# Kernel optimization log

Measured on AMD Instinct MI355X. Metric: run time of the kernel, lower is better.

The kernel has to match this reference:

```python
import jax, jax.numpy as jnp
import numpy as np

OBS, ACT, HID, MIX, TOPK = 64, 16, 256, 16, 4
EPS = 1e-5

def _ln(x, g, b):
    m = jnp.mean(x, axis=-1, keepdims=True)
    v = jnp.mean(jnp.square(x - m), axis=-1, keepdims=True)
    return (x - m) * jax.lax.rsqrt(v + EPS) * g + b

def setup_inputs() -> dict:
    key = jax.random.key(0)
    ks = jax.random.split(key, 12)
    B = 16384
    D = OBS + ACT            # 80
    F = HID * MIX            # 4096
    s = lambda fan_in: 1.0 / np.sqrt(fan_in)
    return {
        "x": jax.random.normal(ks[0], (B, OBS), jnp.float32),
        "a": jax.random.normal(ks[1], (B, ACT), jnp.float32),
        "W1": jax.random.uniform(ks[2], (F, D), jnp.float32, -s(D), s(D)),
        "b1": jnp.zeros((F,), jnp.float32),
        "W2": jax.random.uniform(ks[3], (F, F), jnp.float32, -s(F), s(F)),
        "b2": jnp.zeros((F,), jnp.float32),
        "W3": jax.random.uniform(ks[4], (1, HID), jnp.float32, -s(HID), s(HID)),
        "b3": jnp.zeros((1,), jnp.float32),
        "g1": jnp.ones((F,), jnp.float32),
        "be1": jnp.zeros((F,), jnp.float32),
        "g2": jnp.ones((F,), jnp.float32),
        "be2": jnp.zeros((F,), jnp.float32),
        "Wg": jax.random.uniform(ks[5], (MIX, D), jnp.float32, -s(D), s(D)),
        "bg": jnp.zeros((MIX,), jnp.float32),
    }

def reference(x, a, W1, b1, W2, b2, W3, b3, g1, be1, g2, be2, Wg, bg):
    B = x.shape[0]
    xa = jnp.concatenate([x, a], axis=1)                      # [B, D]
    gate_scores = jax.nn.softmax(xa @ Wg.T + bg, axis=-1)     # [B, MIX]
    topk_vals, topk_idx = jax.lax.top_k(gate_scores, TOPK)    # [B, K]
    # renormalize top-k weights, scatter into dense score tensor
    topk_vals = topk_vals / jnp.sum(topk_vals, axis=-1, keepdims=True)
    scores = jnp.zeros_like(gate_scores).at[
        jnp.arange(B)[:, None], topk_idx].set(topk_vals)      # [B, MIX]
    h = jax.nn.relu(_ln(xa @ W1.T + b1, g1, be1))             # [B, HID*MIX]
    h = jax.nn.relu(_ln(h @ W2.T + b2, g2, be2))              # [B, HID*MIX]
    h = h.reshape(B, HID, MIX)                                # row-major, same as torch
    h = jnp.mean(h * scores[:, None, :], axis=-1)             # [B, HID]
    return h @ W3.T + b3                                      # [B, 1]
```

## Files before the change

kernel.cpp:

```cpp
#include <hip/hip_runtime.h>
#include <stdint.h>

#define OBS 64
#define ACTD 16
#define DIN 80
#define MIX 16
#define FF 4096
#define NB 16384
#define CHUNK 4096
#define KP 96
#define LNEPS 1e-5f

typedef float f32x4 __attribute__((ext_vector_type(4)));
typedef short bf16x8 __attribute__((ext_vector_type(8)));

__device__ __forceinline__ unsigned short f2bf(float f) {
    union { float f; uint32_t u; } v; v.f = f;
    uint32_t u = v.u;
    u += 0x7fff + ((u >> 16) & 1);
    return (unsigned short)(u >> 16);
}
__device__ __forceinline__ float bf2f(unsigned short h) {
    union { uint32_t u; float f; } v; v.u = ((uint32_t)h) << 16;
    return v.f;
}

__global__ __launch_bounds__(256) void k_conv(const float* __restrict__ W,
                                              unsigned short* __restrict__ O, int n4) {
    int i = blockIdx.x * 256 + threadIdx.x;
    if (i >= n4) return;
    float4 v = ((const float4*)W)[i];
    ushort4 o;
    o.x = f2bf(v.x); o.y = f2bf(v.y); o.z = f2bf(v.z); o.w = f2bf(v.w);
    ((ushort4*)O)[i] = o;
}

__global__ __launch_bounds__(256) void k_prep(const float* __restrict__ x, const float* __restrict__ a,
                                              const float* __restrict__ W1, const float* __restrict__ b1,
                                              unsigned short* __restrict__ xab,
                                              unsigned short* __restrict__ W1b) {
    int t = threadIdx.x;
    if (blockIdx.x < 16) {
        int row = blockIdx.x * 256 + t;
        const float4* xp = (const float4*)(x + (size_t)row * OBS);
        unsigned short* o = xab + (size_t)row * KP;
#pragma unroll
        for (int i = 0; i < 16; ++i) {
            float4 v = xp[i];
            ushort4 u; u.x = f2bf(v.x); u.y = f2bf(v.y); u.z = f2bf(v.z); u.w = f2bf(v.w);
            ((ushort4*)o)[i] = u;
        }
        const float4* ap = (const float4*)(a + (size_t)row * ACTD);
#pragma unroll
        for (int i = 0; i < 4; ++i) {
            float4 v = ap[i];
            ushort4 u; u.x = f2bf(v.x); u.y = f2bf(v.y); u.z = f2bf(v.z); u.w = f2bf(v.w);
            ((ushort4*)(o + OBS))[i] = u;
        }
        ushort4 t0; t0.x = 0x3F80; t0.y = 0; t0.z = 0; t0.w = 0;
        ushort4 z;  z.x = 0; z.y = 0; z.z = 0; z.w = 0;
        ((ushort4*)(o + 80))[0] = t0;
        ((ushort4*)(o + 84))[0] = z;
        ((ushort4*)(o + 88))[0] = z;
        ((ushort4*)(o + 92))[0] = z;
    } else {
        int f = (blockIdx.x - 16) * 256 + t;
        const float4* wp = (const float4*)(W1 + (size_t)f * DIN);
        unsigned short* o = W1b + (size_t)f * KP;
#pragma unroll
        for (int i = 0; i < 20; ++i) {
            float4 v = wp[i];
            ushort4 u; u.x = f2bf(v.x); u.y = f2bf(v.y); u.z = f2bf(v.z); u.w = f2bf(v.w);
            ((ushort4*)o)[i] = u;
        }
        ushort4 t0; t0.x = f2bf(b1[f]); t0.y = 0; t0.z = 0; t0.w = 0;
        ushort4 z;  z.x = 0; z.y = 0; z.z = 0; z.w = 0;
        ((ushort4*)(o + 80))[0] = t0;
        ((ushort4*)(o + 84))[0] = z;
        ((ushort4*)(o + 88))[0] = z;
        ((ushort4*)(o + 92))[0] = z;
    }
}

__global__ __launch_bounds__(256) void k_gate(const float* __restrict__ x, const float* __restrict__ a,
                                              const float* __restrict__ Wg, const float* __restrict__ bg,
                                              float* __restrict__ scores) {
    __shared__ float wgs[MIX * DIN];
    __shared__ float bgs[MIX];
    int t = threadIdx.x;
    for (int e = t; e < MIX * DIN; e += 256) wgs[e] = Wg[e];
    if (t < MIX) bgs[t] = bg[t];
    __syncthreads();
    int row = blockIdx.x * 256 + t;
    float xa[DIN];
    const float4* xp = (const float4*)(x + (size_t)row * OBS);
#pragma unroll
    for (int i = 0; i < OBS / 4; ++i) {
        float4 v = xp[i];
        xa[i*4] = v.x; xa[i*4+1] = v.y; xa[i*4+2] = v.z; xa[i*4+3] = v.w;
    }
    const float4* ap = (const float4*)(a + (size_t)row * ACTD);
#pragma unroll
    for (int i = 0; i < ACTD / 4; ++i) {
        float4 v = ap[i];
        xa[OBS+i*4] = v.x; xa[OBS+i*4+1] = v.y; xa[OBS+i*4+2] = v.z; xa[OBS+i*4+3] = v.w;
    }
    double p[MIX];
    double mx = -1e300;
#pragma unroll
    for (int m = 0; m < MIX; ++m) {
        double acc = (double)bgs[m];
#pragma unroll
        for (int k = 0; k < DIN; ++k) acc += (double)xa[k] * (double)wgs[m*DIN + k];
        p[m] = acc;
        if (acc > mx) mx = acc;
    }
#pragma unroll
    for (int m = 0; m < MIX; ++m) p[m] = exp(p[m] - mx);
    unsigned used = 0;
    double s4 = 0.0;
#pragma unroll
    for (int j = 0; j < 4; ++j) {
        int best = 0; double bv = -1.0;
#pragma unroll
        for (int m = 0; m < MIX; ++m)
            if (!((used >> m) & 1) && p[m] > bv) { bv = p[m]; best = m; }
        used |= 1u << best;
        s4 += bv;
    }
    float* so = scores + (size_t)row * MIX;
#pragma unroll
    for (int m = 0; m < MIX; ++m)
        so[m] = ((used >> m) & 1) ? (float)(p[m] / s4) : 0.f;
}

__global__ __launch_bounds__(256) void k_gemm1(const unsigned short* __restrict__ A,
                                               const unsigned short* __restrict__ B,
                                               unsigned short* __restrict__ C,
                                               float* __restrict__ pstats) {
    __shared__ alignas(16) unsigned short As[12288];
    __shared__ alignas(16) unsigned short Bs[12288];
    int t = threadIdx.x;
    int pm = blockIdx.x & 31;
    int pn = blockIdx.x >> 5;
    int lane = t & 63, wid = t >> 6, wm = wid >> 1, wn = wid & 1;
    int l15 = lane & 15, l4 = lane >> 4;

    const unsigned short* Ap = A + (size_t)pm * 128 * KP;
    const unsigned short* Bp = B + (size_t)pn * 128 * KP;

#pragma unroll
    for (int i = 0; i < 6; ++i) {
        int u = i * 256 + t;
        int r = u / 12, s12 = u - r * 12;
        int q = s12 >> 2, s = s12 & 3;
        int goff = r * KP + q * 32 + ((s ^ ((r >> 1) & 3)) * 8);
        __builtin_amdgcn_global_load_lds(
            (const __attribute__((address_space(1))) void*)(Ap + goff),
            (__attribute__((address_space(3))) void*)(As + u * 8), 16, 0, 0);
        __builtin_amdgcn_global_load_lds(
            (const __attribute__((address_space(1))) void*)(Bp + goff),
            (__attribute__((address_space(3))) void*)(Bs + u * 8), 16, 0, 0);
    }
    __syncthreads();

    f32x4 acc[4][4] = {};
#pragma unroll
    for (int q = 0; q < 3; ++q) {
        bf16x8 af[4], bfr[4];
#pragma unroll
        for (int mf = 0; mf < 4; ++mf) {
            int r = wm * 64 + mf * 16 + l15;
            int sl = l4 ^ ((r >> 1) & 3);
            af[mf] = *(const bf16x8*)(As + (r * 12 + q * 4 + sl) * 8);
        }
#pragma unroll
        for (int nf = 0; nf < 4; ++nf) {
            int r = wn * 64 + nf * 16 + l15;
            int sl = l4 ^ ((r >> 1) & 3);
            bfr[nf] = *(const bf16x8*)(Bs + (r * 12 + q * 4 + sl) * 8);
        }
#pragma unroll
        for (int mf = 0; mf < 4; ++mf)
#pragma unroll
            for (int nf = 0; nf < 4; ++nf)
                acc[mf][nf] = __builtin_amdgcn_mfma_f32_16x16x32_bf16(af[mf], bfr[nf], acc[mf][nf], 0, 0, 0);
    }

    int rowbase = pm * 128 + wm * 64 + l4 * 4;
#pragma unroll
    for (int mf = 0; mf < 4; ++mf) {
#pragma unroll
        for (int rr = 0; rr < 4; ++rr) {
            float ss = 0.f, qq = 0.f;
#pragma unroll
            for (int nf = 0; nf < 4; ++nf) {
                float v = acc[mf][nf][rr];
                ss += v; qq += v * v;
            }
#pragma unroll
            for (int mask = 1; mask <= 8; mask <<= 1) {
                ss += __shfl_xor(ss, mask);
                qq += __shfl_xor(qq, mask);
            }
            if (l15 == 0) {
                int row = rowbase + mf * 16 + rr;
                int j = pn * 2 + wn;
                pstats[((size_t)row * 64 + j) * 2 + 0] = ss;
                pstats[((size_t)row * 64 + j) * 2 + 1] = qq;
            }
        }
    }

    __syncthreads();
    unsigned short* tw = As + wid * 1280;
#pragma unroll
    for (int mf = 0; mf < 4; ++mf) {
#pragma unroll
        for (int nf = 0; nf < 4; ++nf)
#pragma unroll
            for (int rr = 0; rr < 4; ++rr) {
                int row16 = l4 * 4 + rr;
                int col = l15 + nf * 16;
                tw[row16 * 80 + col] = f2bf(acc[mf][nf][rr]);
            }
        asm volatile("s_waitcnt lgkmcnt(0)" ::: "memory");
        const bf16x8* rp = (const bf16x8*)(tw + (lane >> 2) * 80 + (lane & 3) * 16);
        bf16x8 v0 = rp[0];
        bf16x8 v1 = rp[1];
        int grow = pm * 128 + wm * 64 + mf * 16 + (lane >> 2);
        int gcol = pn * 128 + wn * 64 + (lane & 3) * 16;
        *(bf16x8*)(C + (size_t)grow * FF + gcol) = v0;
        *(bf16x8*)(C + (size_t)grow * FF + gcol + 8) = v1;
        asm volatile("s_waitcnt lgkmcnt(0)" ::: "memory");
    }
}

__global__ __launch_bounds__(256) void k_ln1(unsigned short* __restrict__ h1,
                                             const float* __restrict__ pstats,
                                             const float* __restrict__ g1, const float* __restrict__ be1) {
    __shared__ float st[8][2];
    int t = threadIdx.x;
    int r0 = blockIdx.x * 8;
    if (t < 8) {
        float s = 0.f, q = 0.f;
        const float* pp = pstats + (size_t)(r0 + t) * 128;
#pragma unroll
        for (int j = 0; j < 64; ++j) { s += pp[j * 2]; q += pp[j * 2 + 1]; }
        float mu = s / (float)FF;
        float var = q / (float)FF - mu * mu;
        st[t][0] = mu;
        st[t][1] = rsqrtf(var + LNEPS);
    }
    __syncthreads();
    int c = t * 16;
    float g[16], b[16];
#pragma unroll
    for (int q = 0; q < 4; ++q) {
        float4 gv = *(const float4*)(g1 + c + q * 4);
        float4 bv = *(const float4*)(be1 + c + q * 4);
        g[q*4] = gv.x; g[q*4+1] = gv.y; g[q*4+2] = gv.z; g[q*4+3] = gv.w;
        b[q*4] = bv.x; b[q*4+1] = bv.y; b[q*4+2] = bv.z; b[q*4+3] = bv.w;
    }
    for (int r = 0; r < 8; ++r) {
        float mu = st[r][0], rs = st[r][1];
        unsigned short* hp = h1 + (size_t)(r0 + r) * FF + c;
        uint4 u0 = *(const uint4*)hp;
        uint4 u1 = *(const uint4*)(hp + 8);
        uint32_t uu[8] = {u0.x, u0.y, u0.z, u0.w, u1.x, u1.y, u1.z, u1.w};
        uint32_t oo[8];
#pragma unroll
        for (int q = 0; q < 8; ++q) {
            float v0 = bf2f((unsigned short)(uu[q] & 0xffff));
            float v1 = bf2f((unsigned short)(uu[q] >> 16));
            float o0 = fmaxf((v0 - mu) * rs * g[q*2]   + b[q*2],   0.f);
            float o1 = fmaxf((v1 - mu) * rs * g[q*2+1] + b[q*2+1], 0.f);
            oo[q] = (uint32_t)f2bf(o0) | ((uint32_t)f2bf(o1) << 16);
        }
        uint4 w0; w0.x = oo[0]; w0.y = oo[1]; w0.z = oo[2]; w0.w = oo[3];
        uint4 w1; w1.x = oo[4]; w1.y = oo[5]; w1.z = oo[6]; w1.w = oo[7];
        *(uint4*)hp = w0;
        *(uint4*)(hp + 8) = w1;
    }
}

__global__ __launch_bounds__(512, 1) void k_gemm2(const unsigned short* __restrict__ A,
                                                  const unsigned short* __restrict__ B,
                                                  unsigned short* __restrict__ C) {
    constexpr int K = FF;
    constexpr int NKT = K / 64;
    __shared__ alignas(16) unsigned short As[2][2][8192];
    __shared__ alignas(16) unsigned short Bs[2][2][8192];

    int t = threadIdx.x;
    int lane = t & 63, wid = t >> 6;
    int wm = wid >> 2, wn = wid & 3;

    int bid = blockIdx.x;
    int xcd = bid & 7, w = bid >> 3;
    int pm = (xcd >> 1) * 4 + (w >> 3);
    int pn = (xcd & 1) * 8 + (w & 7);

    const unsigned short* Ap = A + (size_t)pm * 256 * K;
    const unsigned short* Bp = B + (size_t)pn * 256 * K;

    int l15 = lane & 15, l4 = lane >> 4;
    int slk0 = (l4 ^ (l15 & 7)) * 16;
    int slk1 = ((4 + l4) ^ (l15 & 7)) * 16;
    const char* Abase = (const char*)&As[0][0][0];
    const char* Bbase = (const char*)&Bs[0][0][0];
    const char* afp0 = Abase + wm * 16384 + l15 * 128 + slk0;
    const char* afp1 = Abase + wm * 16384 + l15 * 128 + slk1;
    const char* bfp0 = Bbase + (wn >> 1) * 16384 + (wn & 1) * 8192 + l15 * 128 + slk0;
    const char* bfp1 = Bbase + (wn >> 1) * 16384 + (wn & 1) * 8192 + l15 * 128 + slk1;

    int r0 = t >> 3;
    int swz = ((t & 7) ^ (r0 & 7)) * 8;
    const unsigned short* sA0 = Ap + (size_t)(r0)       * K + swz;
    const unsigned short* sA1 = Ap + (size_t)(64 + r0)  * K + swz;
    const unsigned short* sA2 = Ap + (size_t)(128 + r0) * K + swz;
    const unsigned short* sA3 = Ap + (size_t)(192 + r0) * K + swz;
    const unsigned short* sB0 = Bp + (size_t)(r0)       * K + swz;
    const unsigned short* sB1 = Bp + (size_t)(64 + r0)  * K + swz;
    const unsigned short* sB2 = Bp + (size_t)(128 + r0) * K + swz;
    const unsigned short* sB3 = Bp + (size_t)(192 + r0) * K + swz;
    char* dA = (char*)&As[0][0][0] + t * 16;
    char* dB = (char*)&Bs[0][0][0] + t * 16;

    f32x4 acc[8][4] = {};
    bf16x8 af[4][2], bfr[4][2];

#define STG_A(BUF, HH, p0, p1)                                                              \
    __builtin_amdgcn_global_load_lds((const __attribute__((address_space(1))) void*)(p0),   \
        (__attribute__((address_space(3))) void*)(dA + (BUF)*32768 + (HH)*16384), 16, 0, 0);\
    __builtin_amdgcn_global_load_lds((const __attribute__((address_space(1))) void*)(p1),   \
        (__attribute__((address_space(3))) void*)(dA + (BUF)*32768 + (HH)*16384 + 8192), 16, 0, 0);
#define STG_B(BUF, HH, p0, p1)                                                              \
    __builtin_amdgcn_global_load_lds((const __attribute__((address_space(1))) void*)(p0),   \
        (__attribute__((address_space(3))) void*)(dB + (BUF)*32768 + (HH)*16384), 16, 0, 0);\
    __builtin_amdgcn_global_load_lds((const __attribute__((address_space(1))) void*)(p1),   \
        (__attribute__((address_space(3))) void*)(dB + (BUF)*32768 + (HH)*16384 + 8192), 16, 0, 0);

#define RD_AF(BUF, MH)                                                                      \
    _Pragma("unroll") for (int m = 0; m < 4; ++m) {                                         \
        af[m][0] = *(const bf16x8*)(afp0 + (BUF)*32768 + (MH)*8192 + m*2048);               \
        af[m][1] = *(const bf16x8*)(afp1 + (BUF)*32768 + (MH)*8192 + m*2048);               \
    }
#define RD_BF(BUF)                                                                          \
    _Pragma("unroll") for (int n2 = 0; n2 < 4; ++n2) {                                      \
        bfr[n2][0] = *(const bf16x8*)(bfp0 + (BUF)*32768 + n2*2048);                        \
        bfr[n2][1] = *(const bf16x8*)(bfp1 + (BUF)*32768 + n2*2048);                        \
    }

#define MFMA_Q(MB, NLO)                                                                     \
    __builtin_amdgcn_s_setprio(1);                                                          \
    _Pragma("unroll") for (int kk = 0; kk < 2; ++kk)                                        \
    _Pragma("unroll") for (int m = 0; m < 4; ++m)                                           \
    _Pragma("unroll") for (int n = (NLO); n < (NLO) + 2; ++n)                               \
        acc[(MB)*4 + m][n] = __builtin_amdgcn_mfma_f32_16x16x32_bf16(                       \
            af[m][kk], bfr[n][kk], acc[(MB)*4 + m][n], 0, 0, 0);                            \
    __builtin_amdgcn_s_setprio(0);                                                          \
    __builtin_amdgcn_sched_barrier(0);

#define TILE(BUF, DO_STAGE)                                                                 \
    if (DO_STAGE) { STG_A(1 - (BUF), 0, sA0, sA1) }                                         \
    if (DO_STAGE) asm volatile("s_waitcnt vmcnt(2)" ::: "memory");                          \
    else          asm volatile("s_waitcnt vmcnt(0)" ::: "memory");                          \
    __builtin_amdgcn_s_barrier();                                                           \
    __builtin_amdgcn_sched_barrier(0);                                                      \
    RD_AF(BUF, 0) RD_BF(BUF)                                                                \
    MFMA_Q(0, 0)                                                                            \
    if (DO_STAGE) { STG_A(1 - (BUF), 1, sA2, sA3) }                                         \
    MFMA_Q(0, 2)                                                                            \
    if (DO_STAGE) { STG_B(1 - (BUF), 0, sB0, sB1) }                                         \
    RD_AF(BUF, 1)                                                                           \
    MFMA_Q(1, 0)                                                                            \
    if (DO_STAGE) { STG_B(1 - (BUF), 1, sB2, sB3) }                                         \
    MFMA_Q(1, 2)                                                                            \
    asm volatile("" ::: "memory");                                                          \
    __builtin_amdgcn_s_barrier();                                                           \
    asm volatile("" ::: "memory");                                                          \
    if (DO_STAGE) { sA0 += 64; sA1 += 64; sA2 += 64; sA3 += 64;                             \
                    sB0 += 64; sB1 += 64; sB2 += 64; sB3 += 64; }

    STG_A(0, 0, sA0, sA1) STG_A(0, 1, sA2, sA3)
    STG_B(0, 0, sB0, sB1) STG_B(0, 1, sB2, sB3)
    sA0 += 64; sA1 += 64; sA2 += 64; sA3 += 64;
    sB0 += 64; sB1 += 64; sB2 += 64; sB3 += 64;
    asm volatile("" ::: "memory");

    for (int i = 0; i < NKT / 2 - 1; ++i) {
        TILE(0, true)
        TILE(1, true)
    }
    TILE(0, true)
    TILE(1, false)

#undef STG_A
#undef STG_B
#undef RD_AF
#undef RD_BF
#undef MFMA_Q
#undef TILE

    unsigned short* tw = &As[0][0][0] + wid * 1280;
#pragma unroll
    for (int gm = 0; gm < 8; ++gm) {
#pragma unroll
        for (int gn = 0; gn < 4; ++gn)
#pragma unroll
            for (int rr = 0; rr < 4; ++rr) {
                int row16 = l4 * 4 + rr;
                int col = l15 + gn * 16;
                tw[row16 * 80 + col] = f2bf(acc[gm][gn][rr]);
            }
        asm volatile("s_waitcnt lgkmcnt(0)" ::: "memory");
        const bf16x8* rp = (const bf16x8*)(tw + (lane >> 2) * 80 + (lane & 3) * 16);
        bf16x8 v0 = rp[0];
        bf16x8 v1 = rp[1];
        int grow = pm * 256 + wm * 128 + gm * 16 + (lane >> 2);
        int gcol = pn * 256 + wn * 64 + (lane & 3) * 16;
        *(bf16x8*)(C + (size_t)grow * FF + gcol) = v0;
        *(bf16x8*)(C + (size_t)grow * FF + gcol + 8) = v1;
        asm volatile("s_waitcnt lgkmcnt(0)" ::: "memory");
    }
}

__global__ __launch_bounds__(256) void k_epi(const unsigned short* __restrict__ y2,
                                             const float* __restrict__ scores,
                                             const float* __restrict__ b2,
                                             const float* __restrict__ g2, const float* __restrict__ be2,
                                             const float* __restrict__ W3, const float* __restrict__ b3,
                                             float* __restrict__ out) {
    int row = blockIdx.x, t = threadIdx.x;
    int lane = t & 63, wid = t >> 6;
    __shared__ float sS[MIX];
    __shared__ float rA[4], rB[4];
    __shared__ float stats[2];
    const unsigned short* yp = y2 + (size_t)row * FF + t * 16;
    uint4 u0 = *(const uint4*)yp;
    uint4 u1 = *(const uint4*)(yp + 8);
    float v[16];
    v[0]  = bf2f((unsigned short)(u0.x & 0xffff)); v[1]  = bf2f((unsigned short)(u0.x >> 16));
    v[2]  = bf2f((unsigned short)(u0.y & 0xffff)); v[3]  = bf2f((unsigned short)(u0.y >> 16));
    v[4]  = bf2f((unsigned short)(u0.z & 0xffff)); v[5]  = bf2f((unsigned short)(u0.z >> 16));
    v[6]  = bf2f((unsigned short)(u0.w & 0xffff)); v[7]  = bf2f((unsigned short)(u0.w >> 16));
    v[8]  = bf2f((unsigned short)(u1.x & 0xffff)); v[9]  = bf2f((unsigned short)(u1.x >> 16));
    v[10] = bf2f((unsigned short)(u1.y & 0xffff)); v[11] = bf2f((unsigned short)(u1.y >> 16));
    v[12] = bf2f((unsigned short)(u1.z & 0xffff)); v[13] = bf2f((unsigned short)(u1.z >> 16));
    v[14] = bf2f((unsigned short)(u1.w & 0xffff)); v[15] = bf2f((unsigned short)(u1.w >> 16));
    const float* b2p = b2 + t * 16;
#pragma unroll
    for (int blk = 0; blk < 4; ++blk) {
        float4 q = *(const float4*)(b2p + blk * 4);
        v[blk*4+0] += q.x; v[blk*4+1] += q.y; v[blk*4+2] += q.z; v[blk*4+3] += q.w;
    }
    if (t < MIX) sS[t] = scores[(size_t)row * MIX + t];
    float s = 0.f, sq = 0.f;
#pragma unroll
    for (int j = 0; j < 16; ++j) { s += v[j]; sq += v[j] * v[j]; }
#pragma unroll
    for (int off = 32; off >= 1; off >>= 1) {
        s  += __shfl_down(s, off);
        sq += __shfl_down(sq, off);
    }
    if (lane == 0) { rA[wid] = s; rB[wid] = sq; }
    __syncthreads();
    if (t == 0) {
        float S = rA[0] + rA[1] + rA[2] + rA[3];
        float Q = rB[0] + rB[1] + rB[2] + rB[3];
        float mu = S / (float)FF;
        float var = Q / (float)FF - mu * mu;
        stats[0] = mu;
        stats[1] = rsqrtf(var + LNEPS);
    }
    __syncthreads();
    float mu = stats[0], rs = stats[1];
    const float* gp = g2 + t * 16;
    const float* bp = be2 + t * 16;
    float accum = 0.f;
#pragma unroll
    for (int blk = 0; blk < 4; ++blk) {
        float4 gg = *(const float4*)(gp + blk * 4);
        float4 bb = *(const float4*)(bp + blk * 4);
        float ga[4] = {gg.x, gg.y, gg.z, gg.w};
        float ba[4] = {bb.x, bb.y, bb.z, bb.w};
#pragma unroll
        for (int jj = 0; jj < 4; ++jj) {
            int m = blk * 4 + jj;
            float o = (v[m] - mu) * rs * ga[jj] + ba[jj];
            o = fmaxf(o, 0.f);
            accum += o * sS[m];
        }
    }
    float part = accum * W3[t] * 0.0625f;
#pragma unroll
    for (int off = 32; off >= 1; off >>= 1) part += __shfl_down(part, off);
    if (lane == 0) rA[wid] = part;
    __syncthreads();
    if (t == 0) out[row] = rA[0] + rA[1] + rA[2] + rA[3] + b3[0];
}

extern "C" void kernel_launch(void* const* d_in, const int* in_sizes, int n_in,
                              void* d_out, int out_size, void* d_ws, size_t ws_size,
                              hipStream_t stream) {
    const float* x   = (const float*)d_in[0];
    const float* a   = (const float*)d_in[1];
    const float* W1  = (const float*)d_in[2];
    const float* b1  = (const float*)d_in[3];
    const float* W2  = (const float*)d_in[4];
    const float* b2  = (const float*)d_in[5];
    const float* W3  = (const float*)d_in[6];
    const float* b3  = (const float*)d_in[7];
    const float* g1  = (const float*)d_in[8];
    const float* be1 = (const float*)d_in[9];
    const float* g2  = (const float*)d_in[10];
    const float* be2 = (const float*)d_in[11];
    const float* Wg  = (const float*)d_in[12];
    const float* bg  = (const float*)d_in[13];
    float* out = (float*)d_out;

    char* ws = (char*)d_ws;
    unsigned short* W2b    = (unsigned short*)ws;
    float*          scores = (float*)(ws + 33554432ull);
    unsigned short* h1c    = (unsigned short*)(ws + 34603008ull);
    unsigned short* y2c    = (unsigned short*)(ws + 68157440ull);
    unsigned short* xabc   = (unsigned short*)(ws + 68157440ull);
    unsigned short* W1b    = (unsigned short*)(ws + 68157440ull + 786432ull);
    float*          pstats = (float*)(ws + 68157440ull + 1572864ull);

    k_conv<<<(FF * FF / 4 + 255) / 256, 256, 0, stream>>>(W2, W2b, FF * FF / 4);
    k_gate<<<NB / 256, 256, 0, stream>>>(x, a, Wg, bg, scores);

    for (int c = 0; c < NB / CHUNK; ++c) {
        const float* xc = x + (size_t)c * CHUNK * OBS;
        const float* ac = a + (size_t)c * CHUNK * ACTD;
        const float* sc = scores + (size_t)c * CHUNK * MIX;
        float* oc = out + (size_t)c * CHUNK;
        k_prep<<<32, 256, 0, stream>>>(xc, ac, W1, b1, xabc, W1b);
        k_gemm1<<<(CHUNK / 128) * (FF / 128), 256, 0, stream>>>(xabc, W1b, h1c, pstats);
        k_ln1<<<CHUNK / 8, 256, 0, stream>>>(h1c, pstats, g1, be1);
        k_gemm2<<<(CHUNK / 256) * (FF / 256), 512, 0, stream>>>(h1c, W2b, y2c);
        k_epi<<<CHUNK, 256, 0, stream>>>(y2c, sc, b2, g2, be2, W3, b3, oc);
    }
}
```

Before: 737.4 us.

## Shrink GEMM2 tile to 128x256 with BK=32 for higher occupancy

The second GEMM changes its block tile from 256x256 with a 64-deep K step to 128x256 with a 32-deep K step. That quarters LDS use per block and halves the accumulators per wave, so launch bounds now ask for 4 blocks per CU and the grid doubles. The LDS-staged coalesced epilogue is replaced by direct scattered 2-byte global stores. The intent is more resident waves and more blocks to hide latency, at the cost of lower arithmetic intensity per tile, twice as many barriers per K, and uncoalesced output writes.

After: 846.2 us. +14.7%, slower.

```diff
diff --git a/kernel.cpp b/kernel.cpp
--- a/kernel.cpp
+++ b/kernel.cpp
@@ -284,13 +284,13 @@
     }
 }
 
-__global__ __launch_bounds__(512, 1) void k_gemm2(const unsigned short* __restrict__ A,
+__global__ __launch_bounds__(512, 4) void k_gemm2(const unsigned short* __restrict__ A,
                                                   const unsigned short* __restrict__ B,
                                                   unsigned short* __restrict__ C) {
     constexpr int K = FF;
-    constexpr int NKT = K / 64;
-    __shared__ alignas(16) unsigned short As[2][2][8192];
-    __shared__ alignas(16) unsigned short Bs[2][2][8192];
+    constexpr int NKT = K / 32;
+    __shared__ alignas(16) unsigned short As[2][4096];
+    __shared__ alignas(16) unsigned short Bs[2][8192];
 
     int t = threadIdx.x;
     int lane = t & 63, wid = t >> 6;
@@ -298,132 +298,95 @@
 
     int bid = blockIdx.x;
     int xcd = bid & 7, w = bid >> 3;
-    int pm = (xcd >> 1) * 4 + (w >> 3);
+    int pm = (xcd >> 1) * 8 + (w >> 3);
     int pn = (xcd & 1) * 8 + (w & 7);
 
-    const unsigned short* Ap = A + (size_t)pm * 256 * K;
+    const unsigned short* Ap = A + (size_t)pm * 128 * K;
     const unsigned short* Bp = B + (size_t)pn * 256 * K;
 
     int l15 = lane & 15, l4 = lane >> 4;
-    int slk0 = (l4 ^ (l15 & 7)) * 16;
-    int slk1 = ((4 + l4) ^ (l15 & 7)) * 16;
-    const char* Abase = (const char*)&As[0][0][0];
-    const char* Bbase = (const char*)&Bs[0][0][0];
-    const char* afp0 = Abase + wm * 16384 + l15 * 128 + slk0;
-    const char* afp1 = Abase + wm * 16384 + l15 * 128 + slk1;
-    const char* bfp0 = Bbase + (wn >> 1) * 16384 + (wn & 1) * 8192 + l15 * 128 + slk0;
-    const char* bfp1 = Bbase + (wn >> 1) * 16384 + (wn & 1) * 8192 + l15 * 128 + slk1;
-
-    int r0 = t >> 3;
-    int swz = ((t & 7) ^ (r0 & 7)) * 8;
-    const unsigned short* sA0 = Ap + (size_t)(r0)       * K + swz;
-    const unsigned short* sA1 = Ap + (size_t)(64 + r0)  * K + swz;
-    const unsigned short* sA2 = Ap + (size_t)(128 + r0) * K + swz;
-    const unsigned short* sA3 = Ap + (size_t)(192 + r0) * K + swz;
-    const unsigned short* sB0 = Bp + (size_t)(r0)       * K + swz;
-    const unsigned short* sB1 = Bp + (size_t)(64 + r0)  * K + swz;
-    const unsigned short* sB2 = Bp + (size_t)(128 + r0) * K + swz;
-    const unsigned short* sB3 = Bp + (size_t)(192 + r0) * K + swz;
-    char* dA = (char*)&As[0][0][0] + t * 16;
-    char* dB = (char*)&Bs[0][0][0] + t * 16;
-
-    f32x4 acc[8][4] = {};
-    bf16x8 af[4][2], bfr[4][2];
-
-#define STG_A(BUF, HH, p0, p1)                                                              \
-    __builtin_amdgcn_global_load_lds((const __attribute__((address_space(1))) void*)(p0),   \
-        (__attribute__((address_space(3))) void*)(dA + (BUF)*32768 + (HH)*16384), 16, 0, 0);\
-    __builtin_amdgcn_global_load_lds((const __attribute__((address_space(1))) void*)(p1),   \
-        (__attribute__((address_space(3))) void*)(dA + (BUF)*32768 + (HH)*16384 + 8192), 16, 0, 0);
-#define STG_B(BUF, HH, p0, p1)                                                              \
-    __builtin_amdgcn_global_load_lds((const __attribute__((address_space(1))) void*)(p0),   \
-        (__attribute__((address_space(3))) void*)(dB + (BUF)*32768 + (HH)*16384), 16, 0, 0);\
-    __builtin_amdgcn_global_load_lds((const __attribute__((address_space(1))) void*)(p1),   \
-        (__attribute__((address_space(3))) void*)(dB + (BUF)*32768 + (HH)*16384 + 8192), 16, 0, 0);
-
-#define RD_AF(BUF, MH)                                                                      \
-    _Pragma("unroll") for (int m = 0; m < 4; ++m) {                                         \
-        af[m][0] = *(const bf16x8*)(afp0 + (BUF)*32768 + (MH)*8192 + m*2048);               \
-        af[m][1] = *(const bf16x8*)(afp1 + (BUF)*32768 + (MH)*8192 + m*2048);               \
-    }
-#define RD_BF(BUF)                                                                          \
-    _Pragma("unroll") for (int n2 = 0; n2 < 4; ++n2) {                                      \
-        bfr[n2][0] = *(const bf16x8*)(bfp0 + (BUF)*32768 + n2*2048);                        \
-        bfr[n2][1] = *(const bf16x8*)(bfp1 + (BUF)*32768 + n2*2048);                        \
-    }
-
-#define MFMA_Q(MB, NLO)                                                                     \
+    int slk = (l4 ^ ((l15 >> 1) & 3)) * 16;
+    const char* afp = (const char*)&As[0][0] + wm * 4096 + l15 * 64 + slk;
+    const char* bfp = (const char*)&Bs[0][0] + wn * 4096 + l15 * 64 + slk;
+
+    int r0 = t >> 2;
+    int swz = ((t & 3) ^ ((r0 >> 1) & 3)) * 8;
+    const unsigned short* sA  = Ap + (size_t)r0 * K + swz;
+    const unsigned short* sB0 = Bp + (size_t)r0 * K + swz;
+    const unsigned short* sB1 = Bp + (size_t)(128 + r0) * K + swz;
+    char* dA = (char*)&As[0][0] + t * 16;
+    char* dB = (char*)&Bs[0][0] + t * 16;
+
+    f32x4 acc[4][4] = {};
+    bf16x8 af[4], bfr[4];
+
+#define STG_A2(BUF)                                                                         \
+    __builtin_amdgcn_global_load_lds((const __attribute__((address_space(1))) void*)(sA),   \
+        (__attribute__((address_space(3))) void*)(dA + (BUF)*8192), 16, 0, 0);
+#define STG_B2(BUF, H)                                                                      \
+    __builtin_amdgcn_global_load_lds(                                                       \
+        (const __attribute__((address_space(1))) void*)((H) ? sB1 : sB0),                   \
+        (__attribute__((address_space(3))) void*)(dB + (BUF)*16384 + (H)*8192), 16, 0, 0);
+
+#define RD_AF2(BUF)                                                                         \
+    _Pragma("unroll") for (int m = 0; m < 4; ++m)                                           \
+        af[m] = *(const bf16x8*)(afp + (BUF)*8192 + m*1024);
+#define RD_BF2(BUF, NLO)                                                                    \
+    _Pragma("unroll") for (int n2 = 0; n2 < 2; ++n2)                                        \
+        bfr[(NLO) + n2] = *(const bf16x8*)(bfp + (BUF)*16384 + ((NLO) + n2)*1024);
+
+#define MFMA_Q8(NLO)                                                                        \
     __builtin_amdgcn_s_setprio(1);                                                          \
-    _Pragma("unroll") for (int kk = 0; kk < 2; ++kk)                                        \
     _Pragma("unroll") for (int m = 0; m < 4; ++m)                                           \
     _Pragma("unroll") for (int n = (NLO); n < (NLO) + 2; ++n)                               \
-        acc[(MB)*4 + m][n] = __builtin_amdgcn_mfma_f32_16x16x32_bf16(                       \
-            af[m][kk], bfr[n][kk], acc[(MB)*4 + m][n], 0, 0, 0);                            \
+        acc[m][n] = __builtin_amdgcn_mfma_f32_16x16x32_bf16(af[m], bfr[n], acc[m][n], 0, 0, 0); \
     __builtin_amdgcn_s_setprio(0);                                                          \
     __builtin_amdgcn_sched_barrier(0);
 
-#define TILE(BUF, DO_STAGE)                                                                 \
-    if (DO_STAGE) { STG_A(1 - (BUF), 0, sA0, sA1) }                                         \
-    if (DO_STAGE) asm volatile("s_waitcnt vmcnt(2)" ::: "memory");                          \
+#define TILE2(BUF, DO_STAGE)                                                                \
+    if (DO_STAGE) { STG_A2(1 - (BUF)) }                                                     \
+    if (DO_STAGE) asm volatile("s_waitcnt vmcnt(1)" ::: "memory");                          \
     else          asm volatile("s_waitcnt vmcnt(0)" ::: "memory");                          \
     __builtin_amdgcn_s_barrier();                                                           \
     __builtin_amdgcn_sched_barrier(0);                                                      \
-    RD_AF(BUF, 0) RD_BF(BUF)                                                                \
-    MFMA_Q(0, 0)                                                                            \
-    if (DO_STAGE) { STG_A(1 - (BUF), 1, sA2, sA3) }                                         \
-    MFMA_Q(0, 2)                                                                            \
-    if (DO_STAGE) { STG_B(1 - (BUF), 0, sB0, sB1) }                                         \
-    RD_AF(BUF, 1)                                                                           \
-    MFMA_Q(1, 0)                                                                            \
-    if (DO_STAGE) { STG_B(1 - (BUF), 1, sB2, sB3) }                                         \
-    MFMA_Q(1, 2)                                                                            \
+    RD_AF2(BUF) RD_BF2(BUF, 0)                                                              \
+    MFMA_Q8(0)                                                                              \
+    if (DO_STAGE) { STG_B2(1 - (BUF), 0) }                                                  \
+    RD_BF2(BUF, 2)                                                                          \
+    MFMA_Q8(2)                                                                              \
+    if (DO_STAGE) { STG_B2(1 - (BUF), 1) }                                                  \
     asm volatile("" ::: "memory");                                                          \
     __builtin_amdgcn_s_barrier();                                                           \
     asm volatile("" ::: "memory");                                                          \
-    if (DO_STAGE) { sA0 += 64; sA1 += 64; sA2 += 64; sA3 += 64;                             \
-                    sB0 += 64; sB1 += 64; sB2 += 64; sB3 += 64; }
-
-    STG_A(0, 0, sA0, sA1) STG_A(0, 1, sA2, sA3)
-    STG_B(0, 0, sB0, sB1) STG_B(0, 1, sB2, sB3)
-    sA0 += 64; sA1 += 64; sA2 += 64; sA3 += 64;
-    sB0 += 64; sB1 += 64; sB2 += 64; sB3 += 64;
+    if (DO_STAGE) { sA += 32; sB0 += 32; sB1 += 32; }
+
+    STG_A2(0) STG_B2(0, 0) STG_B2(0, 1)
+    sA += 32; sB0 += 32; sB1 += 32;
     asm volatile("" ::: "memory");
 
     for (int i = 0; i < NKT / 2 - 1; ++i) {
-        TILE(0, true)
-        TILE(1, true)
-    }
-    TILE(0, true)
-    TILE(1, false)
-
-#undef STG_A
-#undef STG_B
-#undef RD_AF
-#undef RD_BF
-#undef MFMA_Q
-#undef TILE
-
-    unsigned short* tw = &As[0][0][0] + wid * 1280;
-#pragma unroll
-    for (int gm = 0; gm < 8; ++gm) {
-#pragma unroll
-        for (int gn = 0; gn < 4; ++gn)
-#pragma unroll
-            for (int rr = 0; rr < 4; ++rr) {
-                int row16 = l4 * 4 + rr;
-                int col = l15 + gn * 16;
-                tw[row16 * 80 + col] = f2bf(acc[gm][gn][rr]);
-            }
-        asm volatile("s_waitcnt lgkmcnt(0)" ::: "memory");
-        const bf16x8* rp = (const bf16x8*)(tw + (lane >> 2) * 80 + (lane & 3) * 16);
-        bf16x8 v0 = rp[0];
-        bf16x8 v1 = rp[1];
-        int grow = pm * 256 + wm * 128 + gm * 16 + (lane >> 2);
-        int gcol = pn * 256 + wn * 64 + (lane & 3) * 16;
-        *(bf16x8*)(C + (size_t)grow * FF + gcol) = v0;
-        *(bf16x8*)(C + (size_t)grow * FF + gcol + 8) = v1;
-        asm volatile("s_waitcnt lgkmcnt(0)" ::: "memory");
-    }
+        TILE2(0, true)
+        TILE2(1, true)
+    }
+    TILE2(0, true)
+    TILE2(1, false)
+
+#undef STG_A2
+#undef STG_B2
+#undef RD_AF2
+#undef RD_BF2
+#undef MFMA_Q8
+#undef TILE2
+
+    int row0 = pm * 128 + wm * 64 + l4 * 4;
+    int col0 = pn * 256 + wn * 64 + l15;
+#pragma unroll
+    for (int m = 0; m < 4; ++m)
+#pragma unroll
+        for (int n = 0; n < 4; ++n)
+#pragma unroll
+            for (int j = 0; j < 4; ++j)
+                C[(size_t)(row0 + m * 16 + j) * FF + col0 + n * 16] = f2bf(acc[m][n][j]);
 }
 
 __global__ __launch_bounds__(256) void k_epi(const unsigned short* __restrict__ y2,
@@ -540,7 +503,7 @@
         k_prep<<<32, 256, 0, stream>>>(xc, ac, W1, b1, xabc, W1b);
         k_gemm1<<<(CHUNK / 128) * (FF / 128), 256, 0, stream>>>(xabc, W1b, h1c, pstats);
         k_ln1<<<CHUNK / 8, 256, 0, stream>>>(h1c, pstats, g1, be1);
-        k_gemm2<<<(CHUNK / 256) * (FF / 256), 512, 0, stream>>>(h1c, W2b, y2c);
+        k_gemm2<<<(CHUNK / 128) * (FF / 256), 512, 0, stream>>>(h1c, W2b, y2c);
         k_epi<<<CHUNK, 256, 0, stream>>>(y2c, sc, b2, g2, be2, W3, b3, oc);
     }
 }
```
